# Kernel optimization log

Measured on AMD Instinct MI355X. Metric: run time of the kernel, lower is better.

The kernel has to match this reference:

```python
import jax, jax.numpy as jnp
import numpy as np

B, T, C, HS = 8, 4096, 1024, 64
HALF = HS // 2
ROPE_BASE = 10000.0


def _rope_tables(t_len, half_dim, base=ROPE_BASE):
    inv_freq = base ** (-jnp.arange(half_dim, dtype=jnp.float32) / half_dim)
    freqs = jnp.arange(t_len, dtype=jnp.float32)[:, None] * inv_freq[None, :]  # (T, D/2)
    return jnp.cos(freqs), jnp.sin(freqs)


def apply_rope(x, cos, sin):
    # x: (B, T, D) with interleaved even/odd pairs; cos/sin: (T, D/2)
    x_even = x[..., ::2]
    x_odd = x[..., 1::2]
    r_even = x_even * cos[None] - x_odd * sin[None]
    r_odd = x_even * sin[None] + x_odd * cos[None]
    # re-interleave
    return jnp.stack([r_even, r_odd], axis=-1).reshape(x.shape)


def setup_inputs() -> dict:
    key = jax.random.key(0)
    kx, kq, kk, kv = jax.random.split(key, 4)
    s = 1.0 / np.sqrt(C)
    cos, sin = _rope_tables(T, HALF)
    return {
        "x": jax.random.normal(kx, (B, T, C), dtype=jnp.float32),
        "cos": cos,
        "sin": sin,
        "Wq": jax.random.normal(kq, (C, HS), dtype=jnp.float32) * s,
        "Wk": jax.random.normal(kk, (C, HS), dtype=jnp.float32) * s,
        "Wv": jax.random.normal(kv, (C, HS), dtype=jnp.float32) * s,
    }


def reference(x, cos, sin, Wq, Wk, Wv):
    # q/k/v projections (bias-free Linear)
    q = jnp.einsum('btc,cd->btd', x, Wq)
    k = jnp.einsum('btc,cd->btd', x, Wk)
    v = jnp.einsum('btc,cd->btd', x, Wv)
    q = apply_rope(q, cos, sin)
    k = apply_rope(k, cos, sin)
    t = x.shape[1]
    scale = 1.0 / jnp.sqrt(jnp.asarray(k.shape[-1], dtype=x.dtype))
    wei = jnp.einsum('bqd,bkd->bqk', q, k) * scale  # (B, T, T)
    causal = jnp.tril(jnp.ones((t, t), dtype=bool))
    wei = jnp.where(causal[None], wei, -jnp.inf)
    wei = jax.nn.softmax(wei, axis=-1)
    # dropout = 0.0 (eval mode)
    return jnp.einsum('bqk,bkd->bqd', wei, v)
```

## Files before the change

### kernel.cpp

```cpp
#include <hip/hip_runtime.h>
#include <hip/hip_bf16.h>

#define BB 8
#define TT 4096
#define CC 1024
#define HS 64

typedef __attribute__((ext_vector_type(8))) __bf16 bf16x8;
typedef __attribute__((ext_vector_type(4))) __bf16 bf16x4;
typedef __attribute__((ext_vector_type(4))) float f32x4;

static __device__ __forceinline__ unsigned pack_bf16(float a, float b) {
    unsigned short ua = __builtin_bit_cast(unsigned short, (__bf16)a);
    unsigned short ub = __builtin_bit_cast(unsigned short, (__bf16)b);
    return (unsigned)ua | ((unsigned)ub << 16);
}

__global__ __launch_bounds__(256) void wprep_kernel(
    const float* __restrict__ Wq, const float* __restrict__ Wk,
    const float* __restrict__ Wv, __bf16* __restrict__ Wt)
{
    int i = blockIdx.x * 256 + threadIdx.x;
    int dr = i >> 10;
    int c  = i & 1023;
    int m  = dr >> 6;
    int d  = dr & 63;
    const float* src = (m == 0) ? Wq : ((m == 1) ? Wk : Wv);
    float v = src[(long)c * HS + d];
    if (m == 0) v *= 0.125f * 1.4426950408889634f;
    Wt[i] = (__bf16)v;
}

__global__ __launch_bounds__(256) void qkv_rope_kernel(
    const float* __restrict__ x,
    const float* __restrict__ cosT,
    const float* __restrict__ sinT,
    const __bf16* __restrict__ Wt,
    __bf16* __restrict__ Qo, __bf16* __restrict__ Ko, __bf16* __restrict__ Vo)
{
    __shared__ __bf16 xs[64][72];
    __shared__ __bf16 Wl[192][72];

    const int tid  = threadIdx.x;
    const int lane = tid & 63;
    const int w    = tid >> 6;
    const int col  = lane & 15;
    const int grp  = lane >> 4;
    const long rowbase = (long)blockIdx.x * 64;

    f32x4 acc[12];
#pragma unroll
    for (int i = 0; i < 12; i++) acc[i] = 0.0f;

    for (int ck = 0; ck < CC; ck += 64) {
        {
            int r = tid >> 2, c0 = (tid & 3) * 16;
            const float4* src = (const float4*)(x + (rowbase + r) * (long)CC + ck + c0);
#pragma unroll
            for (int i = 0; i < 4; i++) {
                float4 v = src[i];
                bf16x4 t;
                t[0] = (__bf16)v.x; t[1] = (__bf16)v.y;
                t[2] = (__bf16)v.z; t[3] = (__bf16)v.w;
                *(bf16x4*)&xs[r][c0 + i * 4] = t;
            }
        }
        {
#pragma unroll
            for (int i = 0; i < 6; i++) {
                int u = i * 256 + tid;
                int dr = u >> 3, cu = (u & 7) * 8;
                bf16x8 v = *(const bf16x8*)(Wt + (long)dr * CC + ck + cu);
                *(bf16x8*)&Wl[dr][cu] = v;
            }
        }
        __syncthreads();
#pragma unroll
        for (int s = 0; s < 2; s++) {
            bf16x8 a = *(const bf16x8*)&xs[w * 16 + col][s * 32 + grp * 8];
#pragma unroll
            for (int nf = 0; nf < 12; nf++) {
                bf16x8 b = *(const bf16x8*)&Wl[nf * 16 + col][s * 32 + grp * 8];
                acc[nf] = __builtin_amdgcn_mfma_f32_16x16x32_bf16(a, b, acc[nf], 0, 0, 0);
            }
        }
        __syncthreads();
    }

#pragma unroll
    for (int r = 0; r < 4; r++) {
        long grow = rowbase + w * 16 + grp * 4 + r;
        int t = (int)(grow & (TT - 1));
        const float* cp = cosT + (long)t * 32;
        const float* sp = sinT + (long)t * 32;
#pragma unroll
        for (int nf = 0; nf < 4; nf++) {
            int ii = nf * 8 + (col >> 1);
            float cs = cp[ii], sn = sp[ii];
            float sgn_sn = (col & 1) ? sn : -sn;
            float qv = acc[nf][r];
            float qp = __shfl_xor(qv, 1);
            float qo = qv * cs + qp * sgn_sn;
            float kv = acc[nf + 4][r];
            float kp = __shfl_xor(kv, 1);
            float ko = kv * cs + kp * sgn_sn;
            long base = grow * HS + nf * 16 + col;
            Qo[base] = (__bf16)qo;
            Ko[base] = (__bf16)ko;
            xs[nf * 16 + col][w * 16 + grp * 4 + r] = (__bf16)acc[nf + 8][r];
        }
    }
    __syncthreads();
    {
        int d = tid >> 2, seg = tid & 3;
        int b  = (int)(rowbase >> 12);
        int t0 = (int)(rowbase & (TT - 1));
        bf16x8 v0 = *(const bf16x8*)&xs[d][seg * 16];
        bf16x8 v1 = *(const bf16x8*)&xs[d][seg * 16 + 8];
        __bf16* dst = Vo + ((size_t)b * 64 + d) * TT + t0 + seg * 16;
        *(bf16x8*)dst = v0;
        *(bf16x8*)(dst + 8) = v1;
    }
}

__global__ __launch_bounds__(256, 3) void attn_kernel(
    const __bf16* __restrict__ Q, const __bf16* __restrict__ K,
    const __bf16* __restrict__ Vt, float* __restrict__ O,
    float* __restrict__ Opart, float* __restrict__ mlbuf)
{
    __shared__ __bf16 Kl[2][64 * 64];
    __shared__ __bf16 Vl[3][64 * 64];
    __shared__ __align__(16) unsigned char plds[4][2048];

    const int tid  = threadIdx.x;
    const int lane = tid & 63;
    const int col  = lane & 15;
    const int g    = lane >> 4;
    const int w    = tid >> 6;

    const int n   = blockIdx.x;
    const int b   = n & 7;
    const int idx = n >> 3;
    int qt, j0, j1, ch;
    bool partial;
    if (idx < 32)      { qt = 32 + idx;  j0 = 0;  j1 = 32;     partial = true;  ch = 0; }
    else if (idx < 64) { qt = idx;       j0 = 32; j1 = qt + 1; partial = true;  ch = 1; }
    else               { qt = 95 - idx;  j0 = 0;  j1 = qt + 1; partial = false; ch = 0; }

    const int qloc = qt * 64 + w * 16 + col;
    const size_t qrow = (size_t)b * TT + qloc;
    bf16x8 qb[2];
#pragma unroll
    for (int s = 0; s < 2; s++)
        qb[s] = *(const bf16x8*)(Q + qrow * HS + s * 32 + g * 8);

    const int r0 = tid >> 3, c0 = tid & 7;
    const int r1 = r0 + 32;
    const __bf16* Kbase = K + (size_t)b * TT * HS;
    const __bf16* Vbase = Vt + (size_t)b * 64 * TT;

#define SWZ(row, cb) (((row) << 6) | (((cb) ^ ((row) & 7)) << 3))

    f32x4 acc[4];
#pragma unroll
    for (int i = 0; i < 4; i++) acc[i] = 0.f;
    float mrun = -3e38f;
    float lsum0 = 0.f, lsum1 = 0.f, lsum2 = 0.f, lsum3 = 0.f;

    unsigned char* pbase = plds[w] + col * 128;
    const int sw = col & 7;

    bf16x8 sk0, sk1, sv0, sv1;
    auto stageLoad = [&](int j) {
        const __bf16* kp = Kbase + (size_t)(j * 64) * HS;
        sk0 = *(const bf16x8*)(kp + r0 * HS + c0 * 8);
        sk1 = *(const bf16x8*)(kp + r1 * HS + c0 * 8);
        const __bf16* vp = Vbase + j * 64;
        sv0 = *(const bf16x8*)(vp + (size_t)r0 * TT + c0 * 8);
        sv1 = *(const bf16x8*)(vp + (size_t)r1 * TT + c0 * 8);
    };
    auto stageWriteK = [&](int kb) {
        *(bf16x8*)&Kl[kb][SWZ(r0, c0)] = sk0;
        *(bf16x8*)&Kl[kb][SWZ(r1, c0)] = sk1;
    };
    auto stageWriteV = [&](int vb) {
        *(bf16x8*)&Vl[vb][SWZ(r0, c0)] = sv0;
        *(bf16x8*)&Vl[vb][SWZ(r1, c0)] = sv1;
    };

    f32x4 sfA[4], sfB[4];

    auto qkPhase = [&](int jv, f32x4 (&SF)[4]) {
        bf16x8 kf[8];
#pragma unroll
        for (int nf = 0; nf < 4; nf++)
#pragma unroll
            for (int s = 0; s < 2; s++)
                kf[nf * 2 + s] = *(const bf16x8*)&Kl[jv & 1][SWZ(nf * 16 + col, s * 4 + g)];
        __builtin_amdgcn_s_setprio(1);
#pragma unroll
        for (int s = 0; s < 2; s++)
#pragma unroll
            for (int nf = 0; nf < 4; nf++)
                SF[nf] = __builtin_amdgcn_mfma_f32_16x16x32_bf16(kf[nf * 2 + s], qb[s], SF[nf], 0, 0, 0);
        __builtin_amdgcn_s_setprio(0);
    };

    auto finPhase = [&](int jv, f32x4 (&SF)[4], int vb) {
        bf16x8 vf[8];
#pragma unroll
        for (int nf = 0; nf < 4; nf++)
#pragma unroll
            for (int s = 0; s < 2; s++)
                vf[nf * 2 + s] = *(const bf16x8*)&Vl[vb][SWZ(nf * 16 + col, s * 4 + g)];
        if (jv == qt) {
#pragma unroll
            for (int nf = 0; nf < 4; nf++)
#pragma unroll
                for (int r = 0; r < 4; r++)
                    if (jv * 64 + nf * 16 + g * 4 + r > qloc) SF[nf][r] = -3e38f;
        }
        float fm[4];
#pragma unroll
        for (int f = 0; f < 4; f++)
            fm[f] = fmaxf(fmaxf(SF[f][0], SF[f][1]), fmaxf(SF[f][2], SF[f][3]));
        float mt = fmaxf(fmaxf(fm[0], fm[1]), fmaxf(fm[2], fm[3]));
        if (!__all(mt <= mrun + 8.0f)) {
            float mg = fmaxf(mt, __shfl_xor(mt, 16));
            mg = fmaxf(mg, __shfl_xor(mg, 32));
            float mn = fmaxf(mrun, mg);
            float al = exp2f(mrun - mn);
            mrun = mn;
            lsum0 *= al; lsum1 *= al; lsum2 *= al; lsum3 *= al;
#pragma unroll
            for (int nf = 0; nf < 4; nf++) acc[nf] *= al;
        }
#pragma unroll
        for (int f = 0; f < 4; f++) {
            float p0 = exp2f(SF[f][0] - mrun);
            float p1 = exp2f(SF[f][1] - mrun);
            float p2 = exp2f(SF[f][2] - mrun);
            float p3 = exp2f(SF[f][3] - mrun);
            SF[f][0] = p0; SF[f][1] = p1; SF[f][2] = p2; SF[f][3] = p3;
            lsum0 += p0; lsum1 += p1; lsum2 += p2; lsum3 += p3;
        }
#pragma unroll
        for (int nf = 0; nf < 4; nf++) {
            uint2 val;
            val.x = pack_bf16(SF[nf][0], SF[nf][1]);
            val.y = pack_bf16(SF[nf][2], SF[nf][3]);
            *(uint2*)(pbase + ((((nf * 2 + (g >> 1)) ^ sw) << 4) | ((g & 1) << 3))) = val;
        }
        __builtin_amdgcn_s_setprio(1);
#pragma unroll
        for (int s = 0; s < 2; s++) {
            bf16x8 pf = *(const bf16x8*)(pbase + (((s * 4 + g) ^ sw) << 4));
#pragma unroll
            for (int nf = 0; nf < 4; nf++)
                acc[nf] = __builtin_amdgcn_mfma_f32_16x16x32_bf16(vf[nf * 2 + s], pf, acc[nf], 0, 0, 0);
        }
        __builtin_amdgcn_s_setprio(0);
    };

    auto iterStep = [&](int jv, f32x4 (&SFq)[4], f32x4 (&SFf)[4], int vb_f) {
        const bool more = (jv + 1 < j1);
        if (more) stageLoad(jv + 1);
        __builtin_amdgcn_sched_barrier(0);
#pragma unroll
        for (int i = 0; i < 4; i++) SFq[i] = 0.f;
        qkPhase(jv, SFq);
        finPhase(jv - 1, SFf, vb_f);
        if (more) {
            stageWriteK((jv + 1) & 1);
            stageWriteV(vb_f + 2 >= 3 ? vb_f - 1 : vb_f + 2);
        }
        __syncthreads();
    };

    stageLoad(j0);
    stageWriteK(j0 & 1);
    const int vb0 = j0 % 3;
    stageWriteV(vb0);
    __syncthreads();

    {
        const bool more = (j0 + 1 < j1);
        if (more) stageLoad(j0 + 1);
        __builtin_amdgcn_sched_barrier(0);
#pragma unroll
        for (int i = 0; i < 4; i++) sfA[i] = 0.f;
        qkPhase(j0, sfA);
        if (more) {
            stageWriteK((j0 + 1) & 1);
            stageWriteV(vb0 + 1 >= 3 ? vb0 - 2 : vb0 + 1);
        }
        __syncthreads();
    }

    int vb_f = vb0;
    int jv = j0 + 1;
    while (jv + 1 < j1) {
        iterStep(jv, sfB, sfA, vb_f);
        vb_f = (vb_f + 1 >= 3) ? vb_f - 2 : vb_f + 1;
        iterStep(jv + 1, sfA, sfB, vb_f);
        vb_f = (vb_f + 1 >= 3) ? vb_f - 2 : vb_f + 1;
        jv += 2;
    }
    bool lastIsB = false;
    if (jv < j1) {
        iterStep(jv, sfB, sfA, vb_f);
        vb_f = (vb_f + 1 >= 3) ? vb_f - 2 : vb_f + 1;
        lastIsB = true;
    }
    if (lastIsB) finPhase(j1 - 1, sfB, vb_f);
    else         finPhase(j1 - 1, sfA, vb_f);

    float ls = (lsum0 + lsum1) + (lsum2 + lsum3);
    ls += __shfl_xor(ls, 16);
    ls += __shfl_xor(ls, 32);

    if (!partial) {
        float rinv = __builtin_amdgcn_rcpf(ls);
        float* orow = O + qrow * HS;
#pragma unroll
        for (int nf = 0; nf < 4; nf++) {
            float4 v;
            v.x = acc[nf][0] * rinv; v.y = acc[nf][1] * rinv;
            v.z = acc[nf][2] * rinv; v.w = acc[nf][3] * rinv;
            *(float4*)(orow + nf * 16 + g * 4) = v;
        }
    } else {
        const int slot = (b * 32 + (qt - 32)) * 2 + ch;
        float* prow = Opart + ((size_t)slot * 64 + w * 16 + col) * 64;
#pragma unroll
        for (int nf = 0; nf < 4; nf++) {
            float4 v;
            v.x = acc[nf][0]; v.y = acc[nf][1];
            v.z = acc[nf][2]; v.w = acc[nf][3];
            *(float4*)(prow + nf * 16 + g * 4) = v;
        }
        if (g == 0) {
            float2 mv = make_float2(mrun, ls);
            *(float2*)(mlbuf + ((size_t)slot * 64 + w * 16 + col) * 2) = mv;
        }
    }
#undef SWZ
}

__global__ __launch_bounds__(256) void combine_kernel(
    const float* __restrict__ Opart, const float* __restrict__ mlbuf,
    float* __restrict__ O)
{
    const int qi = blockIdx.x;
    const int b  = blockIdx.y;
    const int row = threadIdx.x >> 2;
    const int seg = threadIdx.x & 3;
    const int slot0 = (b * 32 + qi) * 2;

    const float* p0 = mlbuf + ((size_t)slot0 * 64 + row) * 2;
    const float* p1 = mlbuf + ((size_t)(slot0 + 1) * 64 + row) * 2;
    float m0 = p0[0], l0 = p0[1];
    float m1 = p1[0], l1 = p1[1];
    float M  = fmaxf(m0, m1);
    float w0 = exp2f(m0 - M), w1 = exp2f(m1 - M);
    float rinv = 1.0f / (l0 * w0 + l1 * w1);
    w0 *= rinv; w1 *= rinv;

    const float4* s0 = (const float4*)(Opart + ((size_t)slot0 * 64 + row) * 64 + seg * 16);
    const float4* s1 = (const float4*)(Opart + ((size_t)(slot0 + 1) * 64 + row) * 64 + seg * 16);
    float4* dst = (float4*)(O + ((size_t)b * TT + (32 + qi) * 64 + row) * 64 + seg * 16);
#pragma unroll
    for (int i = 0; i < 4; i++) {
        float4 a = s0[i], c = s1[i];
        float4 v;
        v.x = a.x * w0 + c.x * w1;
        v.y = a.y * w0 + c.y * w1;
        v.z = a.z * w0 + c.z * w1;
        v.w = a.w * w0 + c.w * w1;
        dst[i] = v;
    }
}

extern "C" void kernel_launch(void* const* d_in, const int* in_sizes, int n_in,
                              void* d_out, int out_size, void* d_ws, size_t ws_size,
                              hipStream_t stream)
{
    const float* x    = (const float*)d_in[0];
    const float* cosT = (const float*)d_in[1];
    const float* sinT = (const float*)d_in[2];
    const float* Wq   = (const float*)d_in[3];
    const float* Wk   = (const float*)d_in[4];
    const float* Wv   = (const float*)d_in[5];
    float* out = (float*)d_out;

    __bf16* Qb = (__bf16*)d_ws;
    __bf16* Kb = Qb + (size_t)BB * TT * HS;
    __bf16* Vb = Kb + (size_t)BB * TT * HS;
    __bf16* Wt = Vb + (size_t)BB * TT * HS;

    const size_t base_bytes = (size_t)3 * BB * TT * HS * 2 + 192 * 1024 * 2;
    float* Opart = (float*)((char*)d_ws + ((base_bytes + 255) & ~(size_t)255));
    float* mlbuf = Opart + (size_t)8 * 32 * 2 * 64 * 64;

    wprep_kernel<<<(192 * 1024) / 256, 256, 0, stream>>>(Wq, Wk, Wv, Wt);
    qkv_rope_kernel<<<(BB * TT) / 64, 256, 0, stream>>>(x, cosT, sinT, Wt, Qb, Kb, Vb);
    attn_kernel<<<768, 256, 0, stream>>>(Qb, Kb, Vb, out, Opart, mlbuf);
    combine_kernel<<<dim3(32, 8), 256, 0, stream>>>(Opart, mlbuf, out);
}
```

Measured before the change: 84.16 us.

## Load V fragments directly from global memory instead of staging through LDS

Removes the triple-buffered V tile in shared memory. Each wave now loads its V MFMA operands straight from global (L2/L1) into registers at the start of each iteration, which saves LDS space and LDS write/read traffic. In exchange, the same V rows are fetched redundantly by all four waves, and the global load latency is exposed within the iteration rather than prefetched one tile ahead. The freed LDS could raise occupancy.

Measured after the change: 121.4 us. 44.2% more time.

```diff
diff --git a/kernel.cpp b/kernel.cpp
--- a/kernel.cpp
+++ b/kernel.cpp
@@ -129,7 +129,6 @@
     float* __restrict__ Opart, float* __restrict__ mlbuf)
 {
     __shared__ __bf16 Kl[2][64 * 64];
-    __shared__ __bf16 Vl[3][64 * 64];
     __shared__ __align__(16) unsigned char plds[4][2048];
 
     const int tid  = threadIdx.x;
@@ -170,22 +169,23 @@
     unsigned char* pbase = plds[w] + col * 128;
     const int sw = col & 7;
 
-    bf16x8 sk0, sk1, sv0, sv1;
+    bf16x8 sk0, sk1;
     auto stageLoad = [&](int j) {
         const __bf16* kp = Kbase + (size_t)(j * 64) * HS;
         sk0 = *(const bf16x8*)(kp + r0 * HS + c0 * 8);
         sk1 = *(const bf16x8*)(kp + r1 * HS + c0 * 8);
-        const __bf16* vp = Vbase + j * 64;
-        sv0 = *(const bf16x8*)(vp + (size_t)r0 * TT + c0 * 8);
-        sv1 = *(const bf16x8*)(vp + (size_t)r1 * TT + c0 * 8);
     };
     auto stageWriteK = [&](int kb) {
         *(bf16x8*)&Kl[kb][SWZ(r0, c0)] = sk0;
         *(bf16x8*)&Kl[kb][SWZ(r1, c0)] = sk1;
     };
-    auto stageWriteV = [&](int vb) {
-        *(bf16x8*)&Vl[vb][SWZ(r0, c0)] = sv0;
-        *(bf16x8*)&Vl[vb][SWZ(r1, c0)] = sv1;
+    auto loadV = [&](int j, bf16x8 (&vf)[8]) {
+#pragma unroll
+        for (int nf = 0; nf < 4; nf++)
+#pragma unroll
+            for (int s = 0; s < 2; s++)
+                vf[nf * 2 + s] = *(const bf16x8*)(Vbase + (size_t)(nf * 16 + col) * TT
+                                                  + j * 64 + s * 32 + g * 8);
     };
 
     f32x4 sfA[4], sfB[4];
@@ -206,13 +206,7 @@
         __builtin_amdgcn_s_setprio(0);
     };
 
-    auto finPhase = [&](int jv, f32x4 (&SF)[4], int vb) {
-        bf16x8 vf[8];
-#pragma unroll
-        for (int nf = 0; nf < 4; nf++)
-#pragma unroll
-            for (int s = 0; s < 2; s++)
-                vf[nf * 2 + s] = *(const bf16x8*)&Vl[vb][SWZ(nf * 16 + col, s * 4 + g)];
+    auto finPhase = [&](int jv, f32x4 (&SF)[4], bf16x8 (&vf)[8]) {
         if (jv == qt) {
 #pragma unroll
             for (int nf = 0; nf < 4; nf++)
@@ -262,25 +256,22 @@
         __builtin_amdgcn_s_setprio(0);
     };
 
-    auto iterStep = [&](int jv, f32x4 (&SFq)[4], f32x4 (&SFf)[4], int vb_f) {
+    auto iterStep = [&](int jv, f32x4 (&SFq)[4], f32x4 (&SFf)[4]) {
         const bool more = (jv + 1 < j1);
+        bf16x8 vf[8];
         if (more) stageLoad(jv + 1);
+        loadV(jv - 1, vf);
         __builtin_amdgcn_sched_barrier(0);
 #pragma unroll
         for (int i = 0; i < 4; i++) SFq[i] = 0.f;
         qkPhase(jv, SFq);
-        finPhase(jv - 1, SFf, vb_f);
-        if (more) {
-            stageWriteK((jv + 1) & 1);
-            stageWriteV(vb_f + 2 >= 3 ? vb_f - 1 : vb_f + 2);
-        }
+        finPhase(jv - 1, SFf, vf);
+        if (more) stageWriteK((jv + 1) & 1);
         __syncthreads();
     };
 
     stageLoad(j0);
     stageWriteK(j0 & 1);
-    const int vb0 = j0 % 3;
-    stageWriteV(vb0);
     __syncthreads();
 
     {
@@ -290,30 +281,27 @@
 #pragma unroll
         for (int i = 0; i < 4; i++) sfA[i] = 0.f;
         qkPhase(j0, sfA);
-        if (more) {
-            stageWriteK((j0 + 1) & 1);
-            stageWriteV(vb0 + 1 >= 3 ? vb0 - 2 : vb0 + 1);
-        }
+        if (more) stageWriteK((j0 + 1) & 1);
         __syncthreads();
     }
 
-    int vb_f = vb0;
     int jv = j0 + 1;
     while (jv + 1 < j1) {
-        iterStep(jv, sfB, sfA, vb_f);
-        vb_f = (vb_f + 1 >= 3) ? vb_f - 2 : vb_f + 1;
-        iterStep(jv + 1, sfA, sfB, vb_f);
-        vb_f = (vb_f + 1 >= 3) ? vb_f - 2 : vb_f + 1;
+        iterStep(jv, sfB, sfA);
+        iterStep(jv + 1, sfA, sfB);
         jv += 2;
     }
     bool lastIsB = false;
     if (jv < j1) {
-        iterStep(jv, sfB, sfA, vb_f);
-        vb_f = (vb_f + 1 >= 3) ? vb_f - 2 : vb_f + 1;
+        iterStep(jv, sfB, sfA);
         lastIsB = true;
     }
-    if (lastIsB) finPhase(j1 - 1, sfB, vb_f);
-    else         finPhase(j1 - 1, sfA, vb_f);
+    {
+        bf16x8 vf[8];
+        loadV(j1 - 1, vf);
+        if (lastIsB) finPhase(j1 - 1, sfB, vf);
+        else         finPhase(j1 - 1, sfA, vf);
+    }
 
     float ls = (lsum0 + lsum1) + (lsum2 + lsum3);
     ls += __shfl_xor(ls, 16);
```
